# Performance work log

Measured on AMD Instinct MI355X. Metric: run time of the kernel, lower is better.

Reference implementation:

```python
import jax, jax.numpy as jnp
import numpy as np

MAX_CHILD = 64  # max trie branching factor (padding width for per-row child windows)


def setup_inputs() -> dict:
    key = jax.random.key(0)
    B, D, V, N = 1024, 1024, 32000, 200000
    k1, k2, k3, k4 = jax.random.split(key, 4)
    x = jax.random.normal(k1, (B, D), dtype=jnp.float32)
    weight = jax.random.normal(k2, (V, D), dtype=jnp.float32) * 0.02
    bias = jax.random.normal(k3, (V,), dtype=jnp.float32) * 0.02
    # Build a consistent CompactCSRTrie: offsets [N+1], tokens/child_nodes [E]
    rng = np.random.default_rng(0)
    deg = rng.integers(1, MAX_CHILD + 1, size=N)
    offsets = np.zeros(N + 1, dtype=np.int32)
    offsets[1:] = np.cumsum(deg)
    E = int(offsets[-1])
    tokens = rng.integers(0, V, size=E).astype(np.int32)
    child_nodes = rng.integers(0, N, size=E).astype(np.int32)
    cur_node = jax.random.randint(k4, (B,), 0, N, dtype=jnp.int32)
    return {
        "x": x,
        "weight": weight,
        "bias": bias,
        "cur_node": cur_node,
        "offsets": jnp.asarray(offsets),
        "tokens": jnp.asarray(tokens),
        "child_nodes": jnp.asarray(child_nodes),
        "step": 1,
    }


def reference(x, weight, bias, cur_node, offsets, tokens, child_nodes, step):
    # Dense GEMM part of the fused kernel: logits = x @ W^T + b  -> [B, V]
    logits = jnp.einsum("bd,vd->bv", x, weight) + bias
    B, V = logits.shape

    # CSR trie traversal: per row, the children of cur_node are
    # tokens[offsets[cur]:offsets[cur+1]] (valid next tokens) and
    # child_nodes[...] (next trie nodes). Gather a padded MAX_CHILD window.
    start = offsets[cur_node]                              # [B]
    deg = offsets[cur_node + 1] - start                    # [B]
    pos = jnp.arange(MAX_CHILD, dtype=start.dtype)         # [C]
    idx = jnp.minimum(start[:, None] + pos[None, :], tokens.shape[0] - 1)  # [B, C]
    valid = pos[None, :] < deg[:, None]                    # [B, C] bool

    tok = tokens[idx]                                      # [B, C] valid token columns
    child = child_nodes[idx]                               # [B, C] next trie nodes

    # Validity masking: only valid child tokens keep their logit, rest -> -inf
    rows = jnp.arange(B)[:, None]
    mask = jnp.zeros((B, V), dtype=bool).at[rows, tok].max(valid)
    masked_logits = jnp.where(mask, logits, -jnp.inf)

    next_nodes = jnp.where(valid, child, -1)               # [B, C], -1 padded
    valid_idxs = jnp.where(valid, tok, -1)                 # [B, C], -1 padded
    return next_nodes, valid_idxs, masked_logits
```

## Files before the change

kernel.cpp:

```cpp
#include <hip/hip_runtime.h>
#include <math.h>

#define B_ 1024
#define D_ 1024
#define V_ 32000
#define MAXC 64
#define HALF_TOK 16000
#define HALF_F4  4000

#define NEG_FILL (-3.0e38f)

typedef float vfloat4 __attribute__((ext_vector_type(4)));

__global__ __launch_bounds__(256, 8) void constrained_linear_kernel(
    const float* __restrict__ x,
    const float* __restrict__ weight,
    const float* __restrict__ bias,
    const int* __restrict__ cur_node,
    const int* __restrict__ offsets,
    const int* __restrict__ tokens,
    const int* __restrict__ child_nodes,
    float* __restrict__ next_nodes,
    float* __restrict__ valid_idxs,
    float* __restrict__ masked_logits)
{
    __shared__ int   ltok[MAXC];
    __shared__ float lval[MAXC];

    const int bid  = blockIdx.x;
    const int b    = bid >> 1;
    const int h    = bid & 1;
    const int tid  = threadIdx.x;
    const int wave = tid >> 6;
    const int lane = tid & 63;

    const int cur = cur_node[b];
    const int start = offsets[cur];
    int deg = offsets[cur + 1] - start;
    if (deg > MAXC) deg = MAXC;

    int tok = -1;
    bool match = false;
    float bv = 0.0f;
    if (lane < deg) {
        tok = tokens[start + lane];
        match = ((unsigned)tok / HALF_TOK) == (unsigned)h;
    }
    if (match) bv = bias[tok];
    if (wave == 0) ltok[lane] = match ? tok : -1;
    const unsigned long long mask = __ballot(match);

    unsigned long long mym = 0;
    {
        unsigned long long m = mask;
        int ord = 0;
        while (m) {
            const unsigned long long bit = m & (~m + 1);
            m &= m - 1;
            if ((ord & 3) == wave) mym |= bit;
            ++ord;
        }
    }

    float4 wA[4];
    int sA = -1, tA = 0;
    if (mym) {
        sA = __builtin_ctzll(mym);
        mym &= mym - 1;
        tA = __shfl(tok, sA);
        const float4* w4 = reinterpret_cast<const float4*>(weight + (size_t)tA * D_);
        #pragma unroll
        for (int k = 0; k < 4; ++k)
            wA[k] = w4[k * 64 + lane];
    }

    if (tid < 32) {
        const int c = h * 32 + tid;
        float nn = -1.0f, vi = -1.0f;
        if (c < deg) {
            const int e = start + c;
            nn = (float)child_nodes[e];
            vi = (float)tokens[e];
        }
        next_nodes[b * MAXC + c] = nn;
        valid_idxs[b * MAXC + c] = vi;
    }

    float* ml_row = masked_logits + (size_t)b * V_;
    vfloat4* ml4 = reinterpret_cast<vfloat4*>(ml_row);
    const vfloat4 sent = {NEG_FILL, NEG_FILL, NEG_FILL, NEG_FILL};
    for (int i = h * HALF_F4 + tid; i < (h + 1) * HALF_F4; i += 256)
        __builtin_nontemporal_store(sent, &ml4[i]);

    const float4* x4 = reinterpret_cast<const float4*>(x + (size_t)b * D_);
    if (sA >= 0) {
        float acc = 0.0f;
        #pragma unroll
        for (int k = 0; k < 4; ++k) {
            const float4 xv = x4[k * 64 + lane];
            acc += wA[k].x * xv.x + wA[k].y * xv.y + wA[k].z * xv.z + wA[k].w * xv.w;
        }
        #pragma unroll
        for (int off = 32; off > 0; off >>= 1)
            acc += __shfl_xor(acc, off);
        if (lane == sA) lval[sA] = acc + bv;
    }
    while (mym) {
        const int s = __builtin_ctzll(mym);
        mym &= mym - 1;
        const int t = __shfl(tok, s);
        const float4* w4 = reinterpret_cast<const float4*>(weight + (size_t)t * D_);
        float acc = 0.0f;
        #pragma unroll
        for (int k = 0; k < 4; ++k) {
            const float4 wv = w4[k * 64 + lane];
            const float4 xv = x4[k * 64 + lane];
            acc += wv.x * xv.x + wv.y * xv.y + wv.z * xv.z + wv.w * xv.w;
        }
        #pragma unroll
        for (int off = 32; off > 0; off >>= 1)
            acc += __shfl_xor(acc, off);
        if (lane == s) lval[s] = acc + bv;
    }

    __syncthreads();

    if (tid < MAXC) {
        const int t = ltok[tid];
        if (t >= 0)
            ml_row[t] = lval[tid];
    }
}

extern "C" void kernel_launch(void* const* d_in, const int* in_sizes, int n_in,
                              void* d_out, int out_size, void* d_ws, size_t ws_size,
                              hipStream_t stream) {
    const float* x           = (const float*)d_in[0];
    const float* weight      = (const float*)d_in[1];
    const float* bias        = (const float*)d_in[2];
    const int*   cur_node    = (const int*)d_in[3];
    const int*   offsets     = (const int*)d_in[4];
    const int*   tokens      = (const int*)d_in[5];
    const int*   child_nodes = (const int*)d_in[6];

    float* out = (float*)d_out;
    float* next_nodes    = out;
    float* valid_idxs    = out + (size_t)B_ * MAXC;
    float* masked_logits = out + 2 * (size_t)B_ * MAXC;

    constrained_linear_kernel<<<B_ * 2, 256, 0, stream>>>(
        x, weight, bias, cur_node, offsets, tokens, child_nodes,
        next_nodes, valid_idxs, masked_logits);
}
```

Measured before the change: 50.58 us.

## Stage row quarter in LDS and write masked logits once per quarter

Each row is now split into four vocabulary quarters instead of two. Each block fills an 8000-float LDS buffer with the sentinel, scatters the computed logits into it, then streams it to global memory with nontemporal stores. This replaces the earlier pattern of a sentinel fill followed by scattered overwrites, so global masked_logits is written once instead of twice. The x row is also hoisted into registers for reuse across tokens. The cost is 32KB of LDS per block, which limits occupancy (launch bounds lowered to 4), plus an extra barrier and doubled redundant per-row setup loads.

```diff
diff --git a/kernel.cpp b/kernel.cpp
--- a/kernel.cpp
+++ b/kernel.cpp
@@ -5,14 +5,15 @@
 #define D_ 1024
 #define V_ 32000
 #define MAXC 64
-#define HALF_TOK 16000
-#define HALF_F4  4000
+#define NQ 4
+#define Q_TOK (V_ / NQ)
+#define Q_F4 (Q_TOK / 4)
 
 #define NEG_FILL (-3.0e38f)
 
 typedef float vfloat4 __attribute__((ext_vector_type(4)));
 
-__global__ __launch_bounds__(256, 8) void constrained_linear_kernel(
+__global__ __launch_bounds__(256, 4) void constrained_linear_kernel(
     const float* __restrict__ x,
     const float* __restrict__ weight,
     const float* __restrict__ bias,
@@ -24,12 +25,12 @@
     float* __restrict__ valid_idxs,
     float* __restrict__ masked_logits)
 {
-    __shared__ int   ltok[MAXC];
-    __shared__ float lval[MAXC];
+    __shared__ vfloat4 lrow[Q_F4];
+    float* lrowf = reinterpret_cast<float*>(lrow);
 
     const int bid  = blockIdx.x;
-    const int b    = bid >> 1;
-    const int h    = bid & 1;
+    const int b    = bid >> 2;
+    const int q    = bid & (NQ - 1);
     const int tid  = threadIdx.x;
     const int wave = tid >> 6;
     const int lane = tid & 63;
@@ -44,10 +45,9 @@
     float bv = 0.0f;
     if (lane < deg) {
         tok = tokens[start + lane];
-        match = ((unsigned)tok / HALF_TOK) == (unsigned)h;
+        match = ((unsigned)tok / Q_TOK) == (unsigned)q;
     }
     if (match) bv = bias[tok];
-    if (wave == 0) ltok[lane] = match ? tok : -1;
     const unsigned long long mask = __ballot(match);
 
     unsigned long long mym = 0;
@@ -62,20 +62,14 @@
         }
     }
 
-    float4 wA[4];
-    int sA = -1, tA = 0;
-    if (mym) {
-        sA = __builtin_ctzll(mym);
-        mym &= mym - 1;
-        tA = __shfl(tok, sA);
-        const float4* w4 = reinterpret_cast<const float4*>(weight + (size_t)tA * D_);
-        #pragma unroll
-        for (int k = 0; k < 4; ++k)
-            wA[k] = w4[k * 64 + lane];
-    }
+    const float4* x4 = reinterpret_cast<const float4*>(x + (size_t)b * D_);
+    float4 xv[4];
+    #pragma unroll
+    for (int k = 0; k < 4; ++k)
+        xv[k] = x4[k * 64 + lane];
 
-    if (tid < 32) {
-        const int c = h * 32 + tid;
+    if (tid < 16) {
+        const int c = q * 16 + tid;
         float nn = -1.0f, vi = -1.0f;
         if (c < deg) {
             const int e = start + c;
@@ -86,25 +80,12 @@
         valid_idxs[b * MAXC + c] = vi;
     }
 
-    float* ml_row = masked_logits + (size_t)b * V_;
-    vfloat4* ml4 = reinterpret_cast<vfloat4*>(ml_row);
     const vfloat4 sent = {NEG_FILL, NEG_FILL, NEG_FILL, NEG_FILL};
-    for (int i = h * HALF_F4 + tid; i < (h + 1) * HALF_F4; i += 256)
-        __builtin_nontemporal_store(sent, &ml4[i]);
+    #pragma unroll
+    for (int i = tid; i < Q_F4; i += 256)
+        lrow[i] = sent;
+    __syncthreads();
 
-    const float4* x4 = reinterpret_cast<const float4*>(x + (size_t)b * D_);
-    if (sA >= 0) {
-        float acc = 0.0f;
-        #pragma unroll
-        for (int k = 0; k < 4; ++k) {
-            const float4 xv = x4[k * 64 + lane];
-            acc += wA[k].x * xv.x + wA[k].y * xv.y + wA[k].z * xv.z + wA[k].w * xv.w;
-        }
-        #pragma unroll
-        for (int off = 32; off > 0; off >>= 1)
-            acc += __shfl_xor(acc, off);
-        if (lane == sA) lval[sA] = acc + bv;
-    }
     while (mym) {
         const int s = __builtin_ctzll(mym);
         mym &= mym - 1;
@@ -114,22 +95,21 @@
         #pragma unroll
         for (int k = 0; k < 4; ++k) {
             const float4 wv = w4[k * 64 + lane];
-            const float4 xv = x4[k * 64 + lane];
-            acc += wv.x * xv.x + wv.y * xv.y + wv.z * xv.z + wv.w * xv.w;
+            acc += wv.x * xv[k].x + wv.y * xv[k].y +
+                   wv.z * xv[k].z + wv.w * xv[k].w;
         }
         #pragma unroll
         for (int off = 32; off > 0; off >>= 1)
             acc += __shfl_xor(acc, off);
-        if (lane == s) lval[s] = acc + bv;
+        if (lane == s)
+            lrowf[tok - q * Q_TOK] = acc + bv;
     }
-
     __syncthreads();
 
-    if (tid < MAXC) {
-        const int t = ltok[tid];
-        if (t >= 0)
-            ml_row[t] = lval[tid];
-    }
+    vfloat4* dst = reinterpret_cast<vfloat4*>(masked_logits + (size_t)b * V_) + q * Q_F4;
+    #pragma unroll
+    for (int i = tid; i < Q_F4; i += 256)
+        __builtin_nontemporal_store(lrow[i], &dst[i]);
 }
 
 extern "C" void kernel_launch(void* const* d_in, const int* in_sizes, int n_in,
@@ -148,7 +128,7 @@
     float* valid_idxs    = out + (size_t)B_ * MAXC;
     float* masked_logits = out + 2 * (size_t)B_ * MAXC;
 
-    constrained_linear_kernel<<<B_ * 2, 256, 0, stream>>>(
+    constrained_linear_kernel<<<B_ * NQ, 256, 0, stream>>>(
         x, weight, bias, cur_node, offsets, tokens, child_nodes,
         next_nodes, valid_idxs, masked_logits);
 }
```

Result: faster. 47.39 us, median of 2 (-6.3%).
